# Optimization experiments

Hardware: AMD Instinct MI355X
Metric: run time of the kernel (lower is better)

## Reference

```python
import jax, jax.numpy as jnp
import numpy as np


def _gcn_conv(x, edge_index, W, b):
    """PyG GCNConv: add self-loops, symmetric normalization, scatter-add aggregation."""
    N = x.shape[0]
    loops = jnp.arange(N, dtype=edge_index.dtype)
    src = jnp.concatenate([edge_index[0], loops])  # [E+N]
    dst = jnp.concatenate([edge_index[1], loops])  # [E+N]
    # degree computed on destination nodes (flow: source_to_target)
    deg = jax.ops.segment_sum(jnp.ones_like(dst, dtype=x.dtype), dst, num_segments=N)
    deg_inv_sqrt = jnp.where(deg > 0, jax.lax.rsqrt(jnp.maximum(deg, 1.0)), 0.0)
    norm = deg_inv_sqrt[src] * deg_inv_sqrt[dst]  # [E+N]
    h = x @ W  # [N, out]
    msg = h[src] * norm[:, None]  # [E+N, out]
    out = jax.ops.segment_sum(msg, dst, num_segments=N)
    return out + b


def setup_inputs() -> dict:
    key = jax.random.key(0)
    k1, k2, k3, k4 = jax.random.split(key, 4)
    N, E, D_IN, D_HID, D_OUT = 100000, 1600000, 128, 128, 64
    x = jax.random.normal(k1, (N, D_IN), dtype=jnp.float32)
    edge_index = jax.random.randint(k2, (2, E), 0, N, dtype=jnp.int64)
    batch = jnp.zeros((N,), dtype=jnp.int64)
    W1 = jax.random.normal(k3, (D_IN, D_HID), dtype=jnp.float32) / np.sqrt(D_IN)
    b1 = jnp.zeros((D_HID,), dtype=jnp.float32)
    W2 = jax.random.normal(k4, (D_HID, D_OUT), dtype=jnp.float32) / np.sqrt(D_HID)
    b2 = jnp.zeros((D_OUT,), dtype=jnp.float32)
    return {"x": x, "edge_index": edge_index, "batch": batch,
            "W1": W1, "b1": b1, "W2": W2, "b2": b2}


def reference(x, edge_index, batch, W1, b1, W2, b2):
    h = _gcn_conv(x, edge_index, W1, b1)
    h = jax.nn.relu(h)
    # dropout is identity at inference (training=False)
    out = _gcn_conv(h, edge_index, W2, b2)
    # original computes F.log_softmax but discards it; returns out
    return out
```

## Files before the change

### kernel.cpp

```cpp
#include <hip/hip_runtime.h>
#include <hip/hip_fp16.h>


#define KDIM 128
#define BSHIFT 9
#define BSIZE 512
#define ECHUNK 2048
#define CAP 10240
#define PACK_SHIFT 20
#define PACK_MASK ((1u << PACK_SHIFT) - 1)

typedef _Float16 h8 __attribute__((ext_vector_type(8)));
typedef float f4v __attribute__((ext_vector_type(4)));

__device__ inline h8 pack8(float4 u, float4 v) {
    h8 r;
    r[0] = (_Float16)u.x; r[1] = (_Float16)u.y; r[2] = (_Float16)u.z; r[3] = (_Float16)u.w;
    r[4] = (_Float16)v.x; r[5] = (_Float16)v.y; r[6] = (_Float16)v.z; r[7] = (_Float16)v.w;
    return r;
}


__launch_bounds__(256) __global__
void prep_kernel(const float* __restrict__ X, const float* __restrict__ W,
                 _Float16* __restrict__ outh,
                 const int* __restrict__ src, const int* __restrict__ dst,
                 int* __restrict__ ecnt, unsigned int* __restrict__ packed_out,
                 int N, int E, int NB, int GB, int EB) {
    __shared__ __align__(16) char shbuf[34816];

    const int t = threadIdx.x;
    const int tm = 2 * min(GB, EB);
    bool isg;
    int bid;
    if ((int)blockIdx.x < tm) {
        isg = !(blockIdx.x & 1);
        bid = blockIdx.x >> 1;
    } else {
        bid = (tm >> 1) + ((int)blockIdx.x - tm);
        isg = (GB > EB);
    }

    if (isg) {
        constexpr int K = KDIM;
        constexpr int KS = K + 8;
        constexpr int DOUT = 128;
        constexpr int NT = DOUT / 16;
        _Float16* Wl = (_Float16*)shbuf;

        const int wave = t >> 6;
        const int lane = t & 63;
        const int l15 = lane & 15;
        const int quad = lane >> 4;

#pragma unroll
        for (int i = t; i < DOUT * (K / 4); i += 256) {
            int n = i & (DOUT - 1);
            int kg = i >> 7;
            union { _Float16 h[4]; uint2 u; } tmp;
#pragma unroll
            for (int j = 0; j < 4; j++)
                tmp.h[j] = (_Float16)W[(size_t)(kg * 4 + j) * DOUT + n];
            *(uint2*)(&Wl[n * KS + kg * 4]) = tmp.u;
        }
        __syncthreads();

        const int rowbase = bid * 128;
        const int row0 = rowbase + wave * 32 + l15;
        const int row1 = row0 + 16;
        const int rc0 = min(row0, N - 1);
        const int rc1 = min(row1, N - 1);

        f4v acc[2][NT];
#pragma unroll
        for (int r = 0; r < 2; r++)
#pragma unroll
            for (int ct = 0; ct < NT; ct++) acc[r][ct] = (f4v)0.0f;

#pragma unroll
        for (int kc = 0; kc < K; kc += 32) {
            const int kof = kc + quad * 8;
            const float* p0 = X + (size_t)rc0 * K + kof;
            const float* p1 = X + (size_t)rc1 * K + kof;
            h8 a0 = pack8(*(const float4*)p0, *(const float4*)(p0 + 4));
            h8 a1 = pack8(*(const float4*)p1, *(const float4*)(p1 + 4));
#pragma unroll
            for (int ct = 0; ct < NT; ct++) {
                h8 b = *(const h8*)(&Wl[(size_t)(ct * 16 + l15) * KS + kof]);
                acc[0][ct] = __builtin_amdgcn_mfma_f32_16x16x32_f16(a0, b, acc[0][ct], 0, 0, 0);
                acc[1][ct] = __builtin_amdgcn_mfma_f32_16x16x32_f16(a1, b, acc[1][ct], 0, 0, 0);
            }
        }

#pragma unroll
        for (int r = 0; r < 2; r++) {
            const int rb = rowbase + wave * 32 + r * 16 + quad * 4;
#pragma unroll
            for (int g = 0; g < 4; g++) {
                int row = rb + g;
                if (row < N) {
                    _Float16* op = outh + (size_t)row * DOUT + l15;
#pragma unroll
                    for (int ct = 0; ct < NT; ct++)
                        op[ct * 16] = (_Float16)acc[r][ct][g];
                }
            }
        }
    } else {
        int* lcnt = (int*)shbuf;
        int* lexc = lcnt + 256;
        int* lbase = lexc + 256;
        unsigned int* lpacked = (unsigned int*)(lbase + 256);
        unsigned char* lbslot = (unsigned char*)(lpacked + ECHUNK);

        lcnt[t] = 0;
        __syncthreads();

        const int base = bid * ECHUNK;
        const int cnt = min(ECHUNK, E - base);

#pragma unroll
        for (int j = 0; j < ECHUNK / 256; j++) {
            int e = base + j * 256 + t;
            if (e < E) atomicAdd(&lcnt[dst[e] >> BSHIFT], 1);
        }
        __syncthreads();

        lexc[t] = lcnt[t];
        __syncthreads();
        for (int off = 1; off < 256; off <<= 1) {
            int x = (t >= off) ? lexc[t - off] : 0;
            __syncthreads();
            if (t >= off) lexc[t] += x;
            __syncthreads();
        }
        lexc[t] = lexc[t] - lcnt[t];

        if (t < NB && lcnt[t]) lbase[t] = t * CAP + atomicAdd(&ecnt[t], lcnt[t]);
        __syncthreads();
        lcnt[t] = lexc[t];
        __syncthreads();

#pragma unroll
        for (int j = 0; j < ECHUNK / 256; j++) {
            int e = base + j * 256 + t;
            if (e < E) {
                int d = dst[e];
                int b = d >> BSHIFT;
                int pos = atomicAdd(&lcnt[b], 1);
                lpacked[pos] = (unsigned int)src[e] | ((unsigned int)(d & (BSIZE - 1)) << PACK_SHIFT);
                lbslot[pos] = (unsigned char)b;
            }
        }
        __syncthreads();

#pragma unroll
        for (int j = 0; j < ECHUNK / 256; j++) {
            int s = j * 256 + t;
            if (s < cnt) {
                int b = lbslot[s];
                int pos = lbase[b] + (s - lexc[b]);
                if (pos < (b + 1) * CAP)
                    packed_out[pos] = lpacked[s];
            }
        }
    }
}


__launch_bounds__(1024) __global__
void bfinal_kernel(const unsigned int* __restrict__ packed, const int* __restrict__ ecnt,
                   int* __restrict__ rowptr, float* __restrict__ dinv,
                   int* __restrict__ ssrc, int N, int E, int NB) {
    __shared__ int ncnt[BSIZE];
    __shared__ int sbuf[BSIZE];
    __shared__ int bsc[256];
    __shared__ int bbase_sh;

    const int t = threadIdx.x;
    const int b = blockIdx.x;

    if (t < 256) bsc[t] = (t < NB) ? min(ecnt[t], CAP) : 0;
    if (t < BSIZE) ncnt[t] = 0;
    __syncthreads();

    const int cnt = min(ecnt[b], CAP);
    const unsigned int* pb = packed + (size_t)b * CAP;
    unsigned int held[CAP / 1024];
#pragma unroll
    for (int j = 0; j < CAP / 1024; j++) {
        int e = t + j * 1024;
        if (e < cnt) {
            unsigned int p = pb[e];
            held[j] = p;
            atomicAdd(&ncnt[p >> PACK_SHIFT], 1);
        }
    }

    __syncthreads();
    for (int off = 1; off < 256; off <<= 1) {
        int x = 0;
        if (t < 256 && t >= off) x = bsc[t - off];
        __syncthreads();
        if (t < 256 && t >= off) bsc[t] += x;
        __syncthreads();
    }
    if (t == 0) bbase_sh = (b == 0) ? 0 : bsc[b - 1];

    int mycnt = 0;
    if (t < BSIZE) {
        mycnt = ncnt[t];
        sbuf[t] = mycnt;
    }
    __syncthreads();
    for (int off = 1; off < BSIZE; off <<= 1) {
        int x = 0;
        if (t < BSIZE && t >= off) x = sbuf[t - off];
        __syncthreads();
        if (t < BSIZE && t >= off) sbuf[t] += x;
        __syncthreads();
    }

    const int gb = bbase_sh;
    if (t < BSIZE) {
        int exc = (t == 0) ? 0 : sbuf[t - 1];
        int node = (b << BSHIFT) + t;
        if (node < N) {
            rowptr[node] = gb + exc;
            dinv[node] = rsqrtf((float)(mycnt + 1));
        }
        ncnt[t] = gb + exc;
    }
    if (t == 0 && b == NB - 1) rowptr[N] = gb + cnt;
    __syncthreads();

#pragma unroll
    for (int j = 0; j < CAP / 1024; j++) {
        int e = t + j * 1024;
        if (e < cnt) {
            unsigned int p = held[j];
            int d = p >> PACK_SHIFT;
            int pos = atomicAdd(&ncnt[d], 1);
            ssrc[pos] = (int)(p & PACK_MASK);
        }
    }
}


__launch_bounds__(512, 8) __global__
void agg_gemm_kernel(const __half* __restrict__ hs, const int* __restrict__ rowptr,
                     const int* __restrict__ ssrc, const float* __restrict__ dinv,
                     const float* __restrict__ bias, const float* __restrict__ W2,
                     _Float16* __restrict__ hs2, int N) {
    constexpr int K = KDIM;
    constexpr int KS = K + 8;
    constexpr int DO2 = 64;
    __shared__ _Float16 W2l[DO2 * KS];
    __shared__ _Float16 o_lds[8][4 * KS];

    const int t = threadIdx.x;

#pragma unroll
    for (int i = t; i < DO2 * (K / 4); i += 512) {
        int n = i & (DO2 - 1);
        int kg = i >> 6;
        union { _Float16 h[4]; uint2 u; } tmp;
#pragma unroll
        for (int j = 0; j < 4; j++)
            tmp.h[j] = (_Float16)W2[(size_t)(kg * 4 + j) * DO2 + n];
        *(uint2*)(&W2l[n * KS + kg * 4]) = tmp.u;
    }
    __syncthreads();

    const int nl = t >> 4;
    const int node = blockIdx.x * 32 + nl;
    const int flane = t & 15;
    const int c0 = flane * 8;

    h8 oh;
    if (node < N) {
        const float di = dinv[node];
        float acc[8];
        {
            uint4 u = *(const uint4*)(hs + (size_t)node * K + c0);
            const __half2* hp = (const __half2*)&u;
#pragma unroll
            for (int q = 0; q < 4; q++) {
                float2 f = __half22float2(hp[q]);
                acc[2 * q]     = di * f.x;
                acc[2 * q + 1] = di * f.y;
            }
        }

        const int e0 = rowptr[node];
        const int e1 = rowptr[node + 1];
        int e = e0;
        for (; e + 4 <= e1; e += 4) {
            int s0 = ssrc[e + 0];
            int s1 = ssrc[e + 1];
            int s2 = ssrc[e + 2];
            int s3 = ssrc[e + 3];
            float d0 = dinv[s0];
            float d1 = dinv[s1];
            float d2 = dinv[s2];
            float d3 = dinv[s3];
            uint4 u0 = *(const uint4*)(hs + (size_t)s0 * K + c0);
            uint4 u1 = *(const uint4*)(hs + (size_t)s1 * K + c0);
            uint4 u2 = *(const uint4*)(hs + (size_t)s2 * K + c0);
            uint4 u3 = *(const uint4*)(hs + (size_t)s3 * K + c0);
            const __half2* p0 = (const __half2*)&u0;
            const __half2* p1 = (const __half2*)&u1;
            const __half2* p2 = (const __half2*)&u2;
            const __half2* p3 = (const __half2*)&u3;
#pragma unroll
            for (int q = 0; q < 4; q++) {
                float2 f0 = __half22float2(p0[q]);
                float2 f1 = __half22float2(p1[q]);
                float2 f2 = __half22float2(p2[q]);
                float2 f3 = __half22float2(p3[q]);
                acc[2 * q]     += d0 * f0.x + d1 * f1.x + d2 * f2.x + d3 * f3.x;
                acc[2 * q + 1] += d0 * f0.y + d1 * f1.y + d2 * f2.y + d3 * f3.y;
            }
        }
        for (; e < e1; e++) {
            int s = ssrc[e];
            float ds = dinv[s];
            uint4 u = *(const uint4*)(hs + (size_t)s * K + c0);
            const __half2* hp = (const __half2*)&u;
#pragma unroll
            for (int q = 0; q < 4; q++) {
                float2 f = __half22float2(hp[q]);
                acc[2 * q]     += ds * f.x;
                acc[2 * q + 1] += ds * f.y;
            }
        }

#pragma unroll
        for (int q = 0; q < 2; q++) {
            float4 bq = *(const float4*)(bias + c0 + 4 * q);
            oh[4 * q + 0] = (_Float16)fmaxf(di * acc[4 * q + 0] + bq.x, 0.f);
            oh[4 * q + 1] = (_Float16)fmaxf(di * acc[4 * q + 1] + bq.y, 0.f);
            oh[4 * q + 2] = (_Float16)fmaxf(di * acc[4 * q + 2] + bq.z, 0.f);
            oh[4 * q + 3] = (_Float16)fmaxf(di * acc[4 * q + 3] + bq.w, 0.f);
        }
    } else {
#pragma unroll
        for (int j = 0; j < 8; j++) oh[j] = (_Float16)0.f;
    }

    const int wv = t >> 6;
    const int a = (t >> 4) & 3;
    *(h8*)(&o_lds[wv][a * KS + c0]) = oh;
    asm volatile("s_waitcnt lgkmcnt(0)" ::: "memory");
    __builtin_amdgcn_sched_barrier(0);

    const int lane = t & 63;
    const int l15 = lane & 15;
    const int quad = lane >> 4;

    f4v acc2[4];
#pragma unroll
    for (int ct = 0; ct < 4; ct++) acc2[ct] = (f4v)0.0f;

#pragma unroll
    for (int kc = 0; kc < K; kc += 32) {
        const int kof = kc + quad * 8;
        h8 afr = *(const h8*)(&o_lds[wv][(l15 & 3) * KS + kof]);
#pragma unroll
        for (int ct = 0; ct < 4; ct++) {
            h8 b = *(const h8*)(&W2l[(size_t)(ct * 16 + l15) * KS + kof]);
            acc2[ct] = __builtin_amdgcn_mfma_f32_16x16x32_f16(afr, b, acc2[ct], 0, 0, 0);
        }
    }

    f4v av = (quad == 0) ? acc2[0] : (quad == 1) ? acc2[1]
           : (quad == 2) ? acc2[2] : acc2[3];
    const int rowbase = blockIdx.x * 32 + wv * 4;
#pragma unroll
    for (int g = 0; g < 4; g++) {
        int r = rowbase + g;
        if (r < N)
            hs2[(size_t)r * DO2 + quad * 16 + l15] = (_Float16)(av[g] * dinv[r]);
    }
}


template <int DOUT, bool RELU, bool HOUT>
__launch_bounds__(256) __global__
void agg_kernel(const __half* __restrict__ hs, const int* __restrict__ rowptr,
                const int* __restrict__ ssrc, const float* __restrict__ dinv,
                const float* __restrict__ bias, void* __restrict__ outv, int N) {
    constexpr int TPN = DOUT / 8;
    const int npb = blockDim.x / TPN;
    const int node = blockIdx.x * npb + threadIdx.x / TPN;
    if (node >= N) return;
    const int lane = threadIdx.x % TPN;
    const int c0 = lane * 8;

    float acc[8];
    {
        uint4 u = *(const uint4*)(hs + (size_t)node * DOUT + c0);
        const __half2* hp = (const __half2*)&u;
#pragma unroll
        for (int q = 0; q < 4; q++) {
            float2 f = __half22float2(hp[q]);
            acc[2 * q] = f.x;
            acc[2 * q + 1] = f.y;
        }
    }

    const int e0 = rowptr[node];
    const int e1 = rowptr[node + 1];
    int e = e0;
    for (; e + 4 <= e1; e += 4) {
        int s0 = ssrc[e + 0];
        int s1 = ssrc[e + 1];
        int s2 = ssrc[e + 2];
        int s3 = ssrc[e + 3];
        uint4 u0 = *(const uint4*)(hs + (size_t)s0 * DOUT + c0);
        uint4 u1 = *(const uint4*)(hs + (size_t)s1 * DOUT + c0);
        uint4 u2 = *(const uint4*)(hs + (size_t)s2 * DOUT + c0);
        uint4 u3 = *(const uint4*)(hs + (size_t)s3 * DOUT + c0);
        const __half2* p0 = (const __half2*)&u0;
        const __half2* p1 = (const __half2*)&u1;
        const __half2* p2 = (const __half2*)&u2;
        const __half2* p3 = (const __half2*)&u3;
#pragma unroll
        for (int q = 0; q < 4; q++) {
            float2 f0 = __half22float2(p0[q]);
            float2 f1 = __half22float2(p1[q]);
            float2 f2 = __half22float2(p2[q]);
            float2 f3 = __half22float2(p3[q]);
            acc[2 * q]     += (f0.x + f1.x) + (f2.x + f3.x);
            acc[2 * q + 1] += (f0.y + f1.y) + (f2.y + f3.y);
        }
    }
    for (; e < e1; e++) {
        int s = ssrc[e];
        uint4 u = *(const uint4*)(hs + (size_t)s * DOUT + c0);
        const __half2* hp = (const __half2*)&u;
#pragma unroll
        for (int q = 0; q < 4; q++) {
            float2 f = __half22float2(hp[q]);
            acc[2 * q] += f.x;
            acc[2 * q + 1] += f.y;
        }
    }

    const float di = dinv[node];
    float o[8];
#pragma unroll
    for (int q = 0; q < 2; q++) {
        float4 bq = *(const float4*)(bias + c0 + 4 * q);
        o[4 * q + 0] = di * acc[4 * q + 0] + bq.x;
        o[4 * q + 1] = di * acc[4 * q + 1] + bq.y;
        o[4 * q + 2] = di * acc[4 * q + 2] + bq.z;
        o[4 * q + 3] = di * acc[4 * q + 3] + bq.w;
    }
    if (RELU) {
#pragma unroll
        for (int j = 0; j < 8; j++) o[j] = fmaxf(o[j], 0.f);
    }
    if (HOUT) {
        union { __half2 h[4]; uint4 u; } pk;
#pragma unroll
        for (int q = 0; q < 4; q++)
            pk.h[q] = __floats2half2_rn(o[2 * q], o[2 * q + 1]);
        *(uint4*)((__half*)outv + (size_t)node * DOUT + c0) = pk.u;
    } else {
        float* op = (float*)outv + (size_t)node * DOUT + c0;
        *(float4*)op = make_float4(o[0], o[1], o[2], o[3]);
        *(float4*)(op + 4) = make_float4(o[4], o[5], o[6], o[7]);
    }
}


extern "C" void kernel_launch(void* const* d_in, const int* in_sizes, int n_in,
                              void* d_out, int out_size, void* d_ws, size_t ws_size,
                              hipStream_t stream) {
    const float* x  = (const float*)d_in[0];
    const int*   ei = (const int*)d_in[1];
    const float* W1 = (const float*)d_in[3];
    const float* b1 = (const float*)d_in[4];
    const float* W2 = (const float*)d_in[5];
    const float* b2 = (const float*)d_in[6];
    float* out = (float*)d_out;

    const int N = in_sizes[0] / KDIM;
    const int E = in_sizes[1] / 2;
    const int* esrc = ei;
    const int* edst = ei + E;
    const int NB = (N + BSIZE - 1) >> BSHIFT;

    char* ws = (char*)d_ws;
    size_t off = 0;
    auto alloc = [&](size_t bytes) {
        size_t p = off;
        off = (off + bytes + 511) & ~(size_t)511;
        return p;
    };
    int*      ecnt    = (int*)(ws + alloc((size_t)NB * 4));
    int*      rowptr  = (int*)(ws + alloc((size_t)(N + 1) * 4));
    float*    dinv    = (float*)(ws + alloc((size_t)N * 4));
    int*      ssrc    = (int*)(ws + alloc((size_t)E * 4));
    _Float16* hs1     = (_Float16*)(ws + alloc((size_t)N * KDIM * 2));
    _Float16* hs2     = (_Float16*)(ws + alloc((size_t)N * 64 * 2));
    unsigned int* packed = (unsigned int*)hs2;
    (void)ws_size; (void)n_in; (void)out_size;

    const int eb = (E + ECHUNK - 1) / ECHUNK;
    const int gb = (N + 127) / 128;

    hipMemsetAsync(ecnt, 0, (size_t)NB * 4, stream);

    prep_kernel<<<gb + eb, 256, 0, stream>>>(x, W1, hs1, esrc, edst, ecnt,
                                             packed, N, E, NB, gb, eb);
    bfinal_kernel<<<NB, 1024, 0, stream>>>(packed, ecnt, rowptr, dinv, ssrc, N, E, NB);

    agg_gemm_kernel<<<(N + 31) / 32, 512, 0, stream>>>(
        (const __half*)hs1, rowptr, ssrc, dinv, b1, W2, hs2, N);

    agg_kernel<64, false, false><<<(N + 31) / 32, 256, 0, stream>>>(
        (const __half*)hs2, rowptr, ssrc, dinv, b2, out, N);
}
```

Before: 246.1 us.

## Split X@W1 GEMM across prep kernels and vectorize edge index loads

New measurement: 254.8 us. 3.5% more time.

```diff
diff --git a/kernel.cpp b/kernel.cpp
--- a/kernel.cpp
+++ b/kernel.cpp
@@ -13,6 +13,8 @@
 typedef _Float16 h8 __attribute__((ext_vector_type(8)));
 typedef float f4v __attribute__((ext_vector_type(4)));
 
+typedef int int4v __attribute__((ext_vector_type(4)));
+
 __device__ inline h8 pack8(float4 u, float4 v) {
     h8 r;
     r[0] = (_Float16)u.x; r[1] = (_Float16)u.y; r[2] = (_Float16)u.z; r[3] = (_Float16)u.w;
@@ -22,11 +24,11 @@
 
 
 __launch_bounds__(256) __global__
-void prep_kernel(const float* __restrict__ X, const float* __restrict__ W,
-                 _Float16* __restrict__ outh,
-                 const int* __restrict__ src, const int* __restrict__ dst,
-                 int* __restrict__ ecnt, unsigned int* __restrict__ packed_out,
-                 int N, int E, int NB, int GB, int EB) {
+void prepA_kernel(const float* __restrict__ X, const float* __restrict__ W,
+                  _Float16* __restrict__ outh,
+                  const int* __restrict__ src, const int* __restrict__ dst,
+                  int* __restrict__ ecnt, unsigned int* __restrict__ packed_out,
+                  int N, int E, int NB, int GB, int EB) {
     __shared__ __align__(16) char shbuf[34816];
 
     const int t = threadIdx.x;
@@ -169,79 +171,152 @@
 
 
 __launch_bounds__(1024) __global__
-void bfinal_kernel(const unsigned int* __restrict__ packed, const int* __restrict__ ecnt,
-                   int* __restrict__ rowptr, float* __restrict__ dinv,
-                   int* __restrict__ ssrc, int N, int E, int NB) {
-    __shared__ int ncnt[BSIZE];
-    __shared__ int sbuf[BSIZE];
-    __shared__ int bsc[256];
-    __shared__ int bbase_sh;
+void prepB_kernel(const unsigned int* __restrict__ packed, const int* __restrict__ ecnt,
+                  int* __restrict__ rowptr, float* __restrict__ dinv,
+                  int* __restrict__ ssrc,
+                  const float* __restrict__ X, const float* __restrict__ W,
+                  _Float16* __restrict__ outh, int RA,
+                  int N, int E, int NB, int GB2) {
+    __shared__ __align__(16) char shbuf[34816];
 
     const int t = threadIdx.x;
-    const int b = blockIdx.x;
-
-    if (t < 256) bsc[t] = (t < NB) ? min(ecnt[t], CAP) : 0;
-    if (t < BSIZE) ncnt[t] = 0;
-    __syncthreads();
-
-    const int cnt = min(ecnt[b], CAP);
-    const unsigned int* pb = packed + (size_t)b * CAP;
-    unsigned int held[CAP / 1024];
-#pragma unroll
-    for (int j = 0; j < CAP / 1024; j++) {
-        int e = t + j * 1024;
-        if (e < cnt) {
-            unsigned int p = pb[e];
-            held[j] = p;
-            atomicAdd(&ncnt[p >> PACK_SHIFT], 1);
-        }
-    }
-
-    __syncthreads();
-    for (int off = 1; off < 256; off <<= 1) {
-        int x = 0;
-        if (t < 256 && t >= off) x = bsc[t - off];
-        __syncthreads();
-        if (t < 256 && t >= off) bsc[t] += x;
-        __syncthreads();
-    }
-    if (t == 0) bbase_sh = (b == 0) ? 0 : bsc[b - 1];
-
-    int mycnt = 0;
-    if (t < BSIZE) {
-        mycnt = ncnt[t];
-        sbuf[t] = mycnt;
-    }
-    __syncthreads();
-    for (int off = 1; off < BSIZE; off <<= 1) {
-        int x = 0;
-        if (t < BSIZE && t >= off) x = sbuf[t - off];
-        __syncthreads();
-        if (t < BSIZE && t >= off) sbuf[t] += x;
-        __syncthreads();
-    }
-
-    const int gb = bbase_sh;
-    if (t < BSIZE) {
-        int exc = (t == 0) ? 0 : sbuf[t - 1];
-        int node = (b << BSHIFT) + t;
-        if (node < N) {
-            rowptr[node] = gb + exc;
-            dinv[node] = rsqrtf((float)(mycnt + 1));
-        }
-        ncnt[t] = gb + exc;
-    }
-    if (t == 0 && b == NB - 1) rowptr[N] = gb + cnt;
-    __syncthreads();
-
-#pragma unroll
-    for (int j = 0; j < CAP / 1024; j++) {
-        int e = t + j * 1024;
-        if (e < cnt) {
-            unsigned int p = held[j];
-            int d = p >> PACK_SHIFT;
-            int pos = atomicAdd(&ncnt[d], 1);
-            ssrc[pos] = (int)(p & PACK_MASK);
+    const int tm = 2 * min(NB, GB2);
+    bool isf;
+    int bid;
+    if ((int)blockIdx.x < tm) {
+        isf = !(blockIdx.x & 1);
+        bid = blockIdx.x >> 1;
+    } else {
+        bid = (tm >> 1) + ((int)blockIdx.x - tm);
+        isf = (NB > GB2);
+    }
+
+    if (isf) {
+        int* ncnt = (int*)shbuf;
+        int* sbuf = ncnt + BSIZE;
+        int* bsc = sbuf + BSIZE;
+        int* bbase_sh = bsc + 256;
+
+        const int b = bid;
+
+        if (t < 256) bsc[t] = (t < NB) ? min(ecnt[t], CAP) : 0;
+        if (t < BSIZE) ncnt[t] = 0;
+        __syncthreads();
+
+        const int cnt = min(ecnt[b], CAP);
+        const unsigned int* pb = packed + (size_t)b * CAP;
+        unsigned int held[CAP / 1024];
+#pragma unroll
+        for (int j = 0; j < CAP / 1024; j++) {
+            int e = t + j * 1024;
+            if (e < cnt) {
+                unsigned int p = pb[e];
+                held[j] = p;
+                atomicAdd(&ncnt[p >> PACK_SHIFT], 1);
+            }
+        }
+
+        __syncthreads();
+        for (int off = 1; off < 256; off <<= 1) {
+            int x = 0;
+            if (t < 256 && t >= off) x = bsc[t - off];
+            __syncthreads();
+            if (t < 256 && t >= off) bsc[t] += x;
+            __syncthreads();
+        }
+        if (t == 0) *bbase_sh = (b == 0) ? 0 : bsc[b - 1];
+
+        int mycnt = 0;
+        if (t < BSIZE) {
+            mycnt = ncnt[t];
+            sbuf[t] = mycnt;
+        }
+        __syncthreads();
+        for (int off = 1; off < BSIZE; off <<= 1) {
+            int x = 0;
+            if (t < BSIZE && t >= off) x = sbuf[t - off];
+            __syncthreads();
+            if (t < BSIZE && t >= off) sbuf[t] += x;
+            __syncthreads();
+        }
+
+        const int gb = *bbase_sh;
+        if (t < BSIZE) {
+            int exc = (t == 0) ? 0 : sbuf[t - 1];
+            int node = (b << BSHIFT) + t;
+            if (node < N) {
+                rowptr[node] = gb + exc;
+                dinv[node] = rsqrtf((float)(mycnt + 1));
+            }
+            ncnt[t] = gb + exc;
+        }
+        if (t == 0 && b == NB - 1) rowptr[N] = gb + cnt;
+        __syncthreads();
+
+#pragma unroll
+        for (int j = 0; j < CAP / 1024; j++) {
+            int e = t + j * 1024;
+            if (e < cnt) {
+                unsigned int p = held[j];
+                int d = p >> PACK_SHIFT;
+                int pos = atomicAdd(&ncnt[d], 1);
+                ssrc[pos] = (int)(p & PACK_MASK);
+            }
+        }
+    } else {
+        constexpr int K = KDIM;
+        constexpr int KS = K + 8;
+        constexpr int DOUT = 128;
+        constexpr int NT = DOUT / 16;
+        _Float16* Wl = (_Float16*)shbuf;
+
+        const int wave = t >> 6;
+        const int lane = t & 63;
+        const int l15 = lane & 15;
+        const int quad = lane >> 4;
+
+#pragma unroll
+        for (int i = t; i < DOUT * (K / 4); i += 1024) {
+            int n = i & (DOUT - 1);
+            int kg = i >> 7;
+            union { _Float16 h[4]; uint2 u; } tmp;
+#pragma unroll
+            for (int j = 0; j < 4; j++)
+                tmp.h[j] = (_Float16)W[(size_t)(kg * 4 + j) * DOUT + n];
+            *(uint2*)(&Wl[n * KS + kg * 4]) = tmp.u;
+        }
+        __syncthreads();
+
+        const int rowbase = RA + bid * 256;
+        const int row0 = rowbase + wave * 16 + l15;
+        const int rc0 = min(row0, N - 1);
+
+        f4v acc[NT];
+#pragma unroll
+        for (int ct = 0; ct < NT; ct++) acc[ct] = (f4v)0.0f;
+
+#pragma unroll
+        for (int kc = 0; kc < K; kc += 32) {
+            const int kof = kc + quad * 8;
+            const float* p0 = X + (size_t)rc0 * K + kof;
+            h8 a0 = pack8(*(const float4*)p0, *(const float4*)(p0 + 4));
+#pragma unroll
+            for (int ct = 0; ct < NT; ct++) {
+                h8 b = *(const h8*)(&Wl[(size_t)(ct * 16 + l15) * KS + kof]);
+                acc[ct] = __builtin_amdgcn_mfma_f32_16x16x32_f16(a0, b, acc[ct], 0, 0, 0);
+            }
+        }
+
+        const int rb = rowbase + wave * 16 + quad * 4;
+#pragma unroll
+        for (int g = 0; g < 4; g++) {
+            int row = rb + g;
+            if (row < N) {
+                _Float16* op = outh + (size_t)row * DOUT + l15;
+#pragma unroll
+                for (int ct = 0; ct < NT; ct++)
+                    op[ct * 16] = (_Float16)acc[ct][g];
+            }
         }
     }
 }
@@ -295,11 +370,22 @@
         const int e0 = rowptr[node];
         const int e1 = rowptr[node + 1];
         int e = e0;
+        const int ealign = min(e1, (e0 + 3) & ~3);
+        for (; e < ealign; e++) {
+            int s = ssrc[e];
+            float ds = dinv[s];
+            uint4 u = *(const uint4*)(hs + (size_t)s * K + c0);
+            const __half2* hp = (const __half2*)&u;
+#pragma unroll
+            for (int q = 0; q < 4; q++) {
+                float2 f = __half22float2(hp[q]);
+                acc[2 * q]     += ds * f.x;
+                acc[2 * q + 1] += ds * f.y;
+            }
+        }
         for (; e + 4 <= e1; e += 4) {
-            int s0 = ssrc[e + 0];
-            int s1 = ssrc[e + 1];
-            int s2 = ssrc[e + 2];
-            int s3 = ssrc[e + 3];
+            int4v sv = *(const int4v*)(ssrc + e);
+            int s0 = sv[0], s1 = sv[1], s2 = sv[2], s3 = sv[3];
             float d0 = dinv[s0];
             float d1 = dinv[s1];
             float d2 = dinv[s2];
@@ -412,11 +498,21 @@
     const int e0 = rowptr[node];
     const int e1 = rowptr[node + 1];
     int e = e0;
+    const int ealign = min(e1, (e0 + 3) & ~3);
+    for (; e < ealign; e++) {
+        int s = ssrc[e];
+        uint4 u = *(const uint4*)(hs + (size_t)s * DOUT + c0);
+        const __half2* hp = (const __half2*)&u;
+#pragma unroll
+        for (int q = 0; q < 4; q++) {
+            float2 f = __half22float2(hp[q]);
+            acc[2 * q] += f.x;
+            acc[2 * q + 1] += f.y;
+        }
+    }
     for (; e + 4 <= e1; e += 4) {
-        int s0 = ssrc[e + 0];
-        int s1 = ssrc[e + 1];
-        int s2 = ssrc[e + 2];
-        int s3 = ssrc[e + 3];
+        int4v sv = *(const int4v*)(ssrc + e);
+        int s0 = sv[0], s1 = sv[1], s2 = sv[2], s3 = sv[3];
         uint4 u0 = *(const uint4*)(hs + (size_t)s0 * DOUT + c0);
         uint4 u1 = *(const uint4*)(hs + (size_t)s1 * DOUT + c0);
         uint4 u2 = *(const uint4*)(hs + (size_t)s2 * DOUT + c0);
@@ -509,13 +605,16 @@
     (void)ws_size; (void)n_in; (void)out_size;
 
     const int eb = (E + ECHUNK - 1) / ECHUNK;
-    const int gb = (N + 127) / 128;
+    const int gbA = (N / 2) / 128;
+    const int RA = gbA * 128;
+    const int gbB = (N - RA + 255) / 256;
 
     hipMemsetAsync(ecnt, 0, (size_t)NB * 4, stream);
 
-    prep_kernel<<<gb + eb, 256, 0, stream>>>(x, W1, hs1, esrc, edst, ecnt,
-                                             packed, N, E, NB, gb, eb);
-    bfinal_kernel<<<NB, 1024, 0, stream>>>(packed, ecnt, rowptr, dinv, ssrc, N, E, NB);
+    prepA_kernel<<<gbA + eb, 256, 0, stream>>>(x, W1, hs1, esrc, edst, ecnt,
+                                               packed, N, E, NB, gbA, eb);
+    prepB_kernel<<<NB + gbB, 1024, 0, stream>>>(packed, ecnt, rowptr, dinv, ssrc,
+                                                x, W1, hs1, RA, N, E, NB, gbB);
 
     agg_gemm_kernel<<<(N + 31) / 32, 512, 0, stream>>>(
         (const __half*)hs1, rowptr, ssrc, dinv, b1, W2, hs2, N);
```
